# Performance work log

Measured on AMD Instinct MI355X. Metric: run time of the kernel, lower is better.

The kernel has to match this reference:

```python
import jax, jax.numpy as jnp
import numpy as np

B, T, D = 2, 2048, 2048
NH, NKV = 16, 4
HD = D // NH  # 128
BASE, TSL = 10000.0, 1024


def rotary_tables(T, hd, base=BASE, tsl=TSL):
    # Matches Rotary.forward with rd == hd (rd=0 in __init__ -> full head dim).
    ar = jnp.arange(0, hd, 2, dtype=jnp.float32) / hd
    if T <= tsl:
        inv = 1.0 / (base ** ar)
    else:
        # NTK-style rescale; note right-assoc exponent in original torch code:
        # 1/(base * (T/tsl) ** ((rd/(rd-2)) ** ar))
        inv = 1.0 / (base * jnp.power(T / tsl, jnp.power(hd / (hd - 2.0), ar)))
    f = jnp.outer(jnp.arange(T, dtype=jnp.float32), inv)  # [T, hd//2]
    cos = jnp.cos(f)[None, :, None, :]  # [1,T,1,hd//2]
    sin = jnp.sin(f)[None, :, None, :]
    return cos, sin


def apply_rope(x, cos, sin):
    # full-dim rope: split halves, rotate
    h = x.shape[-1] // 2
    x1, x2 = x[..., :h], x[..., h:]
    return jnp.concatenate((x1 * cos + x2 * sin, -x1 * sin + x2 * cos), axis=-1)


def rms_norm(x):
    eps = jnp.finfo(x.dtype).eps
    return x * jax.lax.rsqrt(jnp.mean(x * x, axis=-1, keepdims=True) + eps)


def setup_inputs() -> dict:
    key = jax.random.key(0)
    k0, k1, k2, k3, k4 = jax.random.split(key, 5)
    s = 0.02
    return {
        "x": jax.random.normal(k0, (B, T, D), jnp.float32),
        "qw": jax.random.normal(k1, (NH * HD, D), jnp.float32) * s,
        "kw": jax.random.normal(k2, (NKV * HD, D), jnp.float32) * s,
        "vw": jax.random.normal(k3, (NKV * HD, D), jnp.float32) * s,
        "ow": jax.random.normal(k4, (D, D), jnp.float32) * s,
        "qg": jnp.ones((NH,), jnp.float32),
    }


def reference(x, qw, kw, vw, ow, qg):
    Bx, Tx, Dx = x.shape
    q = (x @ qw.T).reshape(Bx, Tx, NH, HD)
    k = (x @ kw.T).reshape(Bx, Tx, NKV, HD)
    v = (x @ vw.T).reshape(Bx, Tx, NKV, HD)
    q = rms_norm(q)
    k = rms_norm(k)
    cos, sin = rotary_tables(Tx, HD)
    q = apply_rope(q, cos, sin) * qg[None, None, :, None]
    k = apply_rope(k, cos, sin)
    # GQA: repeat kv heads
    r = NH // NKV
    k = jnp.repeat(k, r, axis=2)  # [B,T,NH,HD]
    v = jnp.repeat(v, r, axis=2)
    scale = 1.0 / jnp.sqrt(jnp.asarray(HD, q.dtype))
    scores = jnp.einsum("bqhd,bkhd->bhqk", q, k) * scale  # [B,NH,T,T]
    causal = jnp.tril(jnp.ones((Tx, Tx), dtype=bool))
    scores = jnp.where(causal[None, None, :, :], scores, jnp.asarray(-jnp.inf, scores.dtype))
    attn = jax.nn.softmax(scores, axis=-1)
    y = jnp.einsum("bhqk,bkhd->bqhd", attn, v)  # [B,T,NH,HD]
    return y.reshape(Bx, Tx, Dx) @ ow.T
```

## Files before the change

kernel.cpp:

```cpp
#include <hip/hip_runtime.h>
#include <hip/hip_bf16.h>
#include <stdint.h>


typedef __attribute__((ext_vector_type(8))) short short8;
typedef __attribute__((ext_vector_type(4))) float f32x4;

#define GLOAD16(gp, lp) \
  __builtin_amdgcn_global_load_lds((const __attribute__((address_space(1))) void*)(gp), \
                                   (__attribute__((address_space(3))) void*)(lp), 16, 0, 0)

__device__ __forceinline__ float bf2f(unsigned short u) {
  union { unsigned int i; float f; } v; v.i = ((unsigned int)u) << 16; return v.f;
}
__device__ __forceinline__ unsigned short f2bf(float f) {
  union { float fl; unsigned int i; } v; v.fl = f;
  unsigned int r = v.i + 0x7fffu + ((v.i >> 16) & 1u);
  return (unsigned short)(r >> 16);
}

__global__ __launch_bounds__(256) void prep_kernel(
    const float* __restrict__ x, const float* __restrict__ qw,
    const float* __restrict__ kw, const float* __restrict__ vw,
    const float* __restrict__ ow,
    unsigned short* __restrict__ xb, unsigned short* __restrict__ wqkv,
    unsigned short* __restrict__ owb, float* __restrict__ cost, float* __restrict__ sint) {
  const int NX = 2097152;
  const int NW = 1572864;
  const int NO = 1048576;
  const int NT = 131072;
  int tid = blockIdx.x * 256 + threadIdx.x;
  if (tid < NX) {
    float4 v = ((const float4*)x)[tid];
    uint2 o; o.x = (unsigned)f2bf(v.x) | ((unsigned)f2bf(v.y) << 16);
    o.y = (unsigned)f2bf(v.z) | ((unsigned)f2bf(v.w) << 16);
    ((uint2*)xb)[tid] = o;
  } else if (tid < NX + NW) {
    int i = tid - NX; int e = i * 4;
    const float* src = (e < 4194304) ? (qw + e)
                     : (e < 5242880) ? (kw + (e - 4194304))
                                     : (vw + (e - 5242880));
    float4 v = *(const float4*)src;
    uint2 o; o.x = (unsigned)f2bf(v.x) | ((unsigned)f2bf(v.y) << 16);
    o.y = (unsigned)f2bf(v.z) | ((unsigned)f2bf(v.w) << 16);
    ((uint2*)wqkv)[i] = o;
  } else if (tid < NX + NW + NO) {
    int i = tid - NX - NW;
    float4 v = ((const float4*)ow)[i];
    uint2 o; o.x = (unsigned)f2bf(v.x) | ((unsigned)f2bf(v.y) << 16);
    o.y = (unsigned)f2bf(v.z) | ((unsigned)f2bf(v.w) << 16);
    ((uint2*)owb)[i] = o;
  } else if (tid < NX + NW + NO + NT) {
    int i = tid - NX - NW - NO;
    int t = i >> 6, j = i & 63;
    float e = exp2f(0.02272008f * (float)j * (1.0f / 64.0f));
    float inv = 1.0f / (10000.0f * exp2f(e));
    float f = (float)t * inv;
    cost[i] = cosf(f);
    sint[i] = sinf(f);
  }
}

template <int OUTF>
__global__ __launch_bounds__(256) void gemm_bt(const unsigned short* __restrict__ A,
                                               const unsigned short* __restrict__ Bw,
                                               void* __restrict__ Cp,
                                               int M, int N, int K) {
  __shared__ unsigned short a_sm[128 * 64];
  __shared__ unsigned short b_sm[128 * 64];
  const int tid = threadIdx.x;
  const int l = tid & 63, w = tid >> 6;
  const int lane_r = l & 15, lane_g = l >> 4;
  const int wr = w >> 1, wc = w & 1;
  const int m0 = blockIdx.y * 128, n0 = blockIdx.x * 128;

  f32x4 acc[4][4];
#pragma unroll
  for (int i = 0; i < 4; ++i)
#pragma unroll
    for (int j = 0; j < 4; ++j) acc[i][j] = {0.f, 0.f, 0.f, 0.f};

  const unsigned short* gA[4]; const unsigned short* gB[4];
  unsigned short* lA[4]; unsigned short* lB[4];
#pragma unroll
  for (int t = 0; t < 4; ++t) {
    int idx = t * 256 + tid;
    int row = idx >> 3, c = idx & 7;
    int gc = c ^ (row & 7);
    gA[t] = A + (size_t)(m0 + row) * K + gc * 8;
    gB[t] = Bw + (size_t)(n0 + row) * K + gc * 8;
    lA[t] = &a_sm[idx * 8];
    lB[t] = &b_sm[idx * 8];
  }
  int oA[2][4], oB[2][4];
#pragma unroll
  for (int ks = 0; ks < 2; ++ks)
#pragma unroll
    for (int i = 0; i < 4; ++i) {
      int ra = wr * 64 + i * 16 + lane_r;
      oA[ks][i] = ((ra * 64 + ks * 32 + lane_g * 8) * 2) ^ ((ra & 7) << 4);
      int rb = wc * 64 + i * 16 + lane_r;
      oB[ks][i] = ((rb * 64 + ks * 32 + lane_g * 8) * 2) ^ ((rb & 7) << 4);
    }

  for (int kt = 0; kt < K; kt += 64) {
#pragma unroll
    for (int t = 0; t < 4; ++t) {
      GLOAD16(gA[t] + kt, lA[t]);
      GLOAD16(gB[t] + kt, lB[t]);
    }
    __syncthreads();
#pragma unroll
    for (int ks = 0; ks < 2; ++ks) {
      short8 af[4], bfr[4];
#pragma unroll
      for (int i = 0; i < 4; ++i) {
        af[i] = *(const short8*)((const char*)a_sm + oA[ks][i]);
        bfr[i] = *(const short8*)((const char*)b_sm + oB[ks][i]);
      }
#pragma unroll
      for (int i = 0; i < 4; ++i)
#pragma unroll
        for (int j = 0; j < 4; ++j)
          acc[i][j] = __builtin_amdgcn_mfma_f32_16x16x32_bf16(af[i], bfr[j], acc[i][j], 0, 0, 0);
    }
    __syncthreads();
  }
#pragma unroll
  for (int i = 0; i < 4; ++i) {
    int row = m0 + wr * 64 + i * 16 + lane_g * 4;
#pragma unroll
    for (int j = 0; j < 4; ++j) {
      int col = n0 + wc * 64 + j * 16 + lane_r;
#pragma unroll
      for (int r = 0; r < 4; ++r) {
        float v = acc[i][j][r];
        if (OUTF)
          ((float*)Cp)[(size_t)(row + r) * N + col] = v;
        else
          ((unsigned short*)Cp)[(size_t)(row + r) * N + col] = f2bf(v);
      }
    }
  }
}

__global__ __launch_bounds__(256) void normrope_kernel(unsigned short* __restrict__ qkv,
                                                       const float* __restrict__ cost,
                                                       const float* __restrict__ sint,
                                                       const float* __restrict__ qg) {
  const int tid = threadIdx.x, l = tid & 63, w = tid >> 6;
  int row = blockIdx.x * 4 + w;
  int tok = row / 20, hh = row - tok * 20;
  int t = tok & 2047;
  bool isq = hh < 16;
  int col0 = isq ? hh * 128 : 2048 + (hh - 16) * 128;
  unsigned short* p = qkv + (size_t)tok * 3072 + col0 + 2 * l;
  unsigned int u = *(const unsigned int*)p;
  float x0 = bf2f((unsigned short)(u & 0xffffu));
  float x1 = bf2f((unsigned short)(u >> 16));
  float ss = x0 * x0 + x1 * x1;
#pragma unroll
  for (int m = 1; m < 64; m <<= 1) ss += __shfl_xor(ss, m);
  float rn = rsqrtf(ss * (1.0f / 128.0f) + 1.1920928955078125e-07f);
  float n0 = x0 * rn, n1 = x1 * rn;
  float p0 = __shfl_xor(n0, 32);
  float p1 = __shfl_xor(n1, 32);
  int jj = (2 * l) & 63;
  float c0 = cost[t * 64 + jj], c1 = cost[t * 64 + jj + 1];
  float s0 = sint[t * 64 + jj], s1 = sint[t * 64 + jj + 1];
  float o0, o1;
  if (l < 32) { o0 = n0 * c0 + p0 * s0; o1 = n1 * c1 + p1 * s1; }
  else        { o0 = -p0 * s0 + n0 * c0; o1 = -p1 * s1 + n1 * c1; }
  if (isq) { float g = qg[hh] * 0.08838834764831845f; o0 *= g; o1 *= g; }
  *(unsigned int*)p = (unsigned)f2bf(o0) | ((unsigned)f2bf(o1) << 16);
}

__global__ __launch_bounds__(256) void vtrans_kernel(const unsigned short* __restrict__ qkv,
                                                     unsigned short* __restrict__ vtg) {
  __shared__ unsigned short tile[64][132];
  int bid = blockIdx.x;
  int pan = bid & 7, tt = bid >> 3;
  int b = pan >> 2, kvh = pan & 3;
  int t0 = tt * 64;
  const unsigned short* src = qkv + ((size_t)(b * 2048 + t0)) * 3072 + 2560 + kvh * 128;
#pragma unroll
  for (int i = 0; i < 8; ++i) {
    int idx = i * 256 + threadIdx.x;
    int row = idx >> 5, c4 = idx & 31;
    uint2 v = *(const uint2*)(src + (size_t)row * 3072 + c4 * 4);
    *(uint2*)&tile[row][c4 * 4] = v;
  }
  __syncthreads();
  unsigned short* dst = vtg + (size_t)pan * 262144 + t0;
#pragma unroll
  for (int i = 0; i < 8; ++i) {
    int idx = i * 256 + threadIdx.x;
    int d = idx >> 4, tc = idx & 15;
    unsigned short a0 = tile[tc * 4 + 0][d], a1 = tile[tc * 4 + 1][d];
    unsigned short a2 = tile[tc * 4 + 2][d], a3 = tile[tc * 4 + 3][d];
    uint2 o; o.x = (unsigned)a0 | ((unsigned)a1 << 16);
    o.y = (unsigned)a2 | ((unsigned)a3 << 16);
    *(uint2*)(dst + (size_t)d * 2048 + tc * 4) = o;
  }
}

__global__ __launch_bounds__(512) void attn_fa4(const unsigned short* __restrict__ qkv,
                                                const unsigned short* __restrict__ vtg,
                                                unsigned short* __restrict__ y) {
  extern __shared__ char smc[];
  const int tid = threadIdx.x;
  const int l = tid & 63, w = tid >> 6;
  const int lane_r = l & 15, lane_g = l >> 4;

  int n = blockIdx.x;
  int pan = n & 7;
  int b = pan >> 2, kvh = pan & 3;
  int idx2 = n >> 3;
  int h = kvh * 4 + (idx2 & 3);
  int pairIdx = idx2 >> 2;
  const size_t rowbase = (size_t)b * 2048;
  const unsigned short* kvK = qkv + rowbase * 3072;
  const unsigned short* vtp = vtg + (size_t)pan * 262144;

  int kg[2], vg[2], sl[2];
#pragma unroll
  for (int t = 0; t < 2; ++t) {
    int idx = t * 512 + tid;
    { int row = idx >> 4, c = idx & 15, gc = c ^ (row & 7);
      kg[t] = row * 3072 + 2048 + kvh * 128 + gc * 8; }
    { int d = idx >> 3, c = idx & 7, gc = c ^ (d & 7);
      vg[t] = d * 2048 + gc * 8; }
    sl[t] = idx * 16;
  }
  const int swz = (lane_r & 7) << 4;
  int oK[4][4];
#pragma unroll
  for (int ct = 0; ct < 4; ++ct)
#pragma unroll
    for (int ks = 0; ks < 4; ++ks)
      oK[ct][ks] = ((ct * 16 + lane_r) * 256 + ks * 64 + lane_g * 16) ^ swz;
  int oV[2][8];
#pragma unroll
  for (int kk = 0; kk < 2; ++kk)
#pragma unroll
    for (int dt = 0; dt < 8; ++dt)
      oV[kk][dt] = ((dt * 16 + lane_r) * 128 + kk * 64 + lane_g * 16) ^ swz;
  const int pbase = 65536 + w * 2048;
  int pw_off[4];
#pragma unroll
  for (int ct = 0; ct < 4; ++ct)
    pw_off[ct] = pbase + lane_r * 128 + ((ct * 32 + lane_g * 8) ^ swz);
  int pr_off[2];
#pragma unroll
  for (int kk = 0; kk < 2; ++kk)
    pr_off[kk] = pbase + lane_r * 128 + ((kk * 64 + lane_g * 16) ^ swz);

  auto STAGE = [&](int tile, int bufsel) {
    const unsigned short* srcK = kvK + (size_t)tile * 64 * 3072;
    const unsigned short* srcV = vtp + tile * 64;
    char* kd = smc + bufsel * 16384;
    char* vd = smc + 32768 + bufsel * 16384;
#pragma unroll
    for (int t = 0; t < 2; ++t) {
      GLOAD16(srcK + kg[t], kd + sl[t]);
      GLOAD16(srcV + vg[t], vd + sl[t]);
    }
  };

#pragma unroll 1
  for (int phase = 0; phase < 2; ++phase) {
    const int qt = phase ? pairIdx : 15 - pairIdx;
    const int q0 = qt * 128;
    const int nkb = 2 * qt + 2;
    const int wrow0 = q0 + w * 16;
    const int qrow = wrow0 + lane_r;

    STAGE(0, 0);
    short8 qf[4];
#pragma unroll
    for (int ks = 0; ks < 4; ++ks)
      qf[ks] = *(const short8*)(qkv + (rowbase + qrow) * 3072 + h * 128 + ks * 32 + lane_g * 8);

    f32x4 acc[8];
#pragma unroll
    for (int dt = 0; dt < 8; ++dt) acc[dt] = {0.f, 0.f, 0.f, 0.f};
    float mrun = -1e30f, lrun = 0.f;

    __syncthreads();

#pragma unroll 1
    for (int kb = 0; kb < nkb; ++kb) {
      const int cur = kb & 1;
      if (kb + 1 < nkb) STAGE(kb + 1, cur ^ 1);
      const int j0 = kb * 64;
      const bool active = (j0 <= wrow0 + 15);
      if (active) {
        const int kbb = cur * 16384;
        f32x4 s[4];
#pragma unroll
        for (int ct = 0; ct < 4; ++ct) s[ct] = {0.f, 0.f, 0.f, 0.f};
        __builtin_amdgcn_s_setprio(1);
#pragma unroll
        for (int ct = 0; ct < 4; ++ct)
#pragma unroll
          for (int ks = 0; ks < 4; ++ks) {
            short8 kf = *(const short8*)(smc + kbb + oK[ct][ks]);
            s[ct] = __builtin_amdgcn_mfma_f32_16x16x32_bf16(kf, qf[ks], s[ct], 0, 0, 0);
          }
        __builtin_amdgcn_s_setprio(0);
        if (j0 + 63 > wrow0) {
#pragma unroll
          for (int ct = 0; ct < 4; ++ct) {
            int kg0 = j0 + ct * 16 + lane_g * 4;
#pragma unroll
            for (int r = 0; r < 4; ++r)
              if (kg0 + r > qrow) s[ct][r] = -1e30f;
          }
        }
        float mx = s[0][0];
#pragma unroll
        for (int ct = 0; ct < 4; ++ct)
#pragma unroll
          for (int r = 0; r < 4; ++r) mx = fmaxf(mx, s[ct][r]);
        mx = fmaxf(mx, __shfl_xor(mx, 16));
        mx = fmaxf(mx, __shfl_xor(mx, 32));
        float mn = fmaxf(mrun, mx);
        float corr = __expf(mrun - mn);
        mrun = mn;
        float rs = 0.f;
#pragma unroll
        for (int ct = 0; ct < 4; ++ct)
#pragma unroll
          for (int r = 0; r < 4; ++r) {
            float e = __expf(s[ct][r] - mn);
            s[ct][r] = e; rs += e;
          }
        rs += __shfl_xor(rs, 16);
        rs += __shfl_xor(rs, 32);
        lrun = lrun * corr + rs;
#pragma unroll
        for (int ct = 0; ct < 4; ++ct) {
          uint2 pv;
          pv.x = (unsigned)f2bf(s[ct][0]) | ((unsigned)f2bf(s[ct][1]) << 16);
          pv.y = (unsigned)f2bf(s[ct][2]) | ((unsigned)f2bf(s[ct][3]) << 16);
          *(uint2*)(smc + pw_off[ct]) = pv;
        }
#pragma unroll
        for (int dt = 0; dt < 8; ++dt)
#pragma unroll
          for (int r = 0; r < 4; ++r) acc[dt][r] *= corr;
        short8 pf[2];
        pf[0] = *(const short8*)(smc + pr_off[0]);
        pf[1] = *(const short8*)(smc + pr_off[1]);
        const int vbase = 32768 + cur * 16384;
        __builtin_amdgcn_s_setprio(1);
#pragma unroll
        for (int kk = 0; kk < 2; ++kk)
#pragma unroll
          for (int dt = 0; dt < 8; ++dt) {
            short8 vf = *(const short8*)(smc + vbase + oV[kk][dt]);
            acc[dt] = __builtin_amdgcn_mfma_f32_16x16x32_bf16(vf, pf[kk], acc[dt], 0, 0, 0);
          }
        __builtin_amdgcn_s_setprio(0);
      }
      __syncthreads();
    }
    float linv = 1.0f / lrun;
    unsigned short* yrow = y + (rowbase + qrow) * 2048 + h * 128;
#pragma unroll
    for (int dt = 0; dt < 8; ++dt) {
      uint2 o;
      o.x = (unsigned)f2bf(acc[dt][0] * linv) | ((unsigned)f2bf(acc[dt][1] * linv) << 16);
      o.y = (unsigned)f2bf(acc[dt][2] * linv) | ((unsigned)f2bf(acc[dt][3] * linv) << 16);
      *(uint2*)(yrow + dt * 16 + lane_g * 4) = o;
    }
  }
}

extern "C" void kernel_launch(void* const* d_in, const int* in_sizes, int n_in,
                              void* d_out, int out_size, void* d_ws, size_t ws_size,
                              hipStream_t stream) {
  (void)in_sizes; (void)n_in; (void)out_size; (void)ws_size;
  const float* x  = (const float*)d_in[0];
  const float* qw = (const float*)d_in[1];
  const float* kw = (const float*)d_in[2];
  const float* vw = (const float*)d_in[3];
  const float* ow = (const float*)d_in[4];
  const float* qg = (const float*)d_in[5];

  char* ws = (char*)d_ws;
  unsigned short* xb   = (unsigned short*)(ws + 0);
  unsigned short* vtg  = (unsigned short*)(ws + 0);
  unsigned short* wqkv = (unsigned short*)(ws + 16777216);
  unsigned short* owb  = (unsigned short*)(ws + 29360128);
  unsigned short* qkvb = (unsigned short*)(ws + 37748736);
  unsigned short* y    = (unsigned short*)(ws + 62914560);
  float* cost          = (float*)(ws + 79691776);
  float* sint          = (float*)(ws + 80216064);

  prep_kernel<<<18944, 256, 0, stream>>>(x, qw, kw, vw, ow, xb, wqkv, owb, cost, sint);
  gemm_bt<0><<<dim3(3072 / 128, 4096 / 128), 256, 0, stream>>>(xb, wqkv, qkvb, 4096, 3072, 2048);
  normrope_kernel<<<20480, 256, 0, stream>>>(qkvb, cost, sint, qg);
  vtrans_kernel<<<256, 256, 0, stream>>>(qkvb, vtg);
  attn_fa4<<<256, 512, 81920, stream>>>(qkvb, vtg, y);
  gemm_bt<1><<<dim3(2048 / 128, 4096 / 128), 256, 0, stream>>>(y, owb, d_out, 4096, 2048, 2048);
}
```

Baseline: 228.0 us.

## Replace GEMM with 256x128-tile, 512-thread, triple-buffered pipelined kernel

Replaces the simple single-buffered 128x128 bf16 GEMM with a 256x128-tile, 8-wave kernel. It uses a three-stage LDS ring with global_load_lds prefetch two K-steps ahead, manual vmcnt waits and a single barrier per step. Workgroup IDs are remapped in chunks of eight, apparently to improve cache locality across CUs. MFMA sections run at raised priority. The goal is to hide global load latency and remove the per-iteration double barrier, at the cost of 144KB dynamic LDS per block, which allows only one block per CU.

```diff
diff --git a/kernel.cpp b/kernel.cpp
--- a/kernel.cpp
+++ b/kernel.cpp
@@ -62,17 +62,22 @@
 }
 
 template <int OUTF>
-__global__ __launch_bounds__(256) void gemm_bt(const unsigned short* __restrict__ A,
-                                               const unsigned short* __restrict__ Bw,
-                                               void* __restrict__ Cp,
-                                               int M, int N, int K) {
-  __shared__ unsigned short a_sm[128 * 64];
-  __shared__ unsigned short b_sm[128 * 64];
+__global__ __launch_bounds__(512) void gemm_bt2(const unsigned short* __restrict__ A,
+                                                const unsigned short* __restrict__ Bw,
+                                                void* __restrict__ Cp,
+                                                int MT, int NT, int N, int K) {
+  extern __shared__ char smc[];
   const int tid = threadIdx.x;
   const int l = tid & 63, w = tid >> 6;
   const int lane_r = l & 15, lane_g = l >> 4;
   const int wr = w >> 1, wc = w & 1;
-  const int m0 = blockIdx.y * 128, n0 = blockIdx.x * 128;
+
+  int nwg = MT * NT, qch = nwg >> 3;
+  int orig = blockIdx.x;
+  int wgid = (orig & 7) * qch + (orig >> 3);
+  int by = wgid % MT;
+  int bx = wgid / MT;
+  const int m0 = by * 256, n0 = bx * 128;
 
   f32x4 acc[4][4];
 #pragma unroll
@@ -80,51 +85,71 @@
 #pragma unroll
     for (int j = 0; j < 4; ++j) acc[i][j] = {0.f, 0.f, 0.f, 0.f};
 
-  const unsigned short* gA[4]; const unsigned short* gB[4];
-  unsigned short* lA[4]; unsigned short* lB[4];
+  const unsigned short* gA[4]; int lA[4];
 #pragma unroll
   for (int t = 0; t < 4; ++t) {
-    int idx = t * 256 + tid;
-    int row = idx >> 3, c = idx & 7;
-    int gc = c ^ (row & 7);
+    int idx = t * 512 + tid;
+    int row = idx >> 3, c = idx & 7, gc = c ^ (row & 7);
     gA[t] = A + (size_t)(m0 + row) * K + gc * 8;
+    lA[t] = idx * 16;
+  }
+  const unsigned short* gB[2]; int lB[2];
+#pragma unroll
+  for (int t = 0; t < 2; ++t) {
+    int idx = t * 512 + tid;
+    int row = idx >> 3, c = idx & 7, gc = c ^ (row & 7);
     gB[t] = Bw + (size_t)(n0 + row) * K + gc * 8;
-    lA[t] = &a_sm[idx * 8];
-    lB[t] = &b_sm[idx * 8];
-  }
-  int oA[2][4], oB[2][4];
-#pragma unroll
-  for (int ks = 0; ks < 2; ++ks)
-#pragma unroll
-    for (int i = 0; i < 4; ++i) {
+    lB[t] = idx * 16;
+  }
+  int oA[4][2], oB[4][2];
+#pragma unroll
+  for (int i = 0; i < 4; ++i)
+#pragma unroll
+    for (int ks = 0; ks < 2; ++ks) {
       int ra = wr * 64 + i * 16 + lane_r;
-      oA[ks][i] = ((ra * 64 + ks * 32 + lane_g * 8) * 2) ^ ((ra & 7) << 4);
+      oA[i][ks] = (ra * 128 + ks * 64 + lane_g * 16) ^ ((ra & 7) << 4);
       int rb = wc * 64 + i * 16 + lane_r;
-      oB[ks][i] = ((rb * 64 + ks * 32 + lane_g * 8) * 2) ^ ((rb & 7) << 4);
+      oB[i][ks] = (rb * 128 + ks * 64 + lane_g * 16) ^ ((rb & 7) << 4);
     }
 
-  for (int kt = 0; kt < K; kt += 64) {
-#pragma unroll
-    for (int t = 0; t < 4; ++t) {
-      GLOAD16(gA[t] + kt, lA[t]);
-      GLOAD16(gB[t] + kt, lB[t]);
-    }
-    __syncthreads();
-#pragma unroll
-    for (int ks = 0; ks < 2; ++ks) {
-      short8 af[4], bfr[4];
-#pragma unroll
-      for (int i = 0; i < 4; ++i) {
-        af[i] = *(const short8*)((const char*)a_sm + oA[ks][i]);
-        bfr[i] = *(const short8*)((const char*)b_sm + oB[ks][i]);
+  auto STAGE = [&](int kt, int bsel) {
+    char* kd = smc + bsel * 49152;
+    char* bd = kd + 32768;
+#pragma unroll
+    for (int t = 0; t < 4; ++t) GLOAD16(gA[t] + kt, kd + lA[t]);
+#pragma unroll
+    for (int t = 0; t < 2; ++t) GLOAD16(gB[t] + kt, bd + lB[t]);
+  };
+
+  const int NS = K >> 6;
+  STAGE(0, 0);
+  STAGE(64, 1);
+#pragma unroll 1
+  for (int s = 0; s < NS; ++s) {
+    if (s + 1 < NS) asm volatile("s_waitcnt vmcnt(6)" ::: "memory");
+    else            asm volatile("s_waitcnt vmcnt(0)" ::: "memory");
+    __builtin_amdgcn_s_barrier();
+    __builtin_amdgcn_sched_barrier(0);
+    if (s + 2 < NS) STAGE((s + 2) * 64, (s + 2) % 3);
+    const char* ab = smc + (s % 3) * 49152;
+    const char* bb = ab + 32768;
+    short8 af[4][2], bf[4][2];
+#pragma unroll
+    for (int i = 0; i < 4; ++i)
+#pragma unroll
+      for (int ks = 0; ks < 2; ++ks) {
+        af[i][ks] = *(const short8*)(ab + oA[i][ks]);
+        bf[i][ks] = *(const short8*)(bb + oB[i][ks]);
       }
-#pragma unroll
-      for (int i = 0; i < 4; ++i)
-#pragma unroll
-        for (int j = 0; j < 4; ++j)
-          acc[i][j] = __builtin_amdgcn_mfma_f32_16x16x32_bf16(af[i], bfr[j], acc[i][j], 0, 0, 0);
-    }
-    __syncthreads();
+    __builtin_amdgcn_s_setprio(1);
+#pragma unroll
+    for (int i = 0; i < 4; ++i)
+#pragma unroll
+      for (int j = 0; j < 4; ++j)
+#pragma unroll
+        for (int ks = 0; ks < 2; ++ks)
+          acc[i][j] = __builtin_amdgcn_mfma_f32_16x16x32_bf16(af[i][ks], bf[j][ks], acc[i][j], 0, 0, 0);
+    __builtin_amdgcn_s_setprio(0);
   }
 #pragma unroll
   for (int i = 0; i < 4; ++i) {
@@ -399,9 +424,9 @@
   float* sint          = (float*)(ws + 80216064);
 
   prep_kernel<<<18944, 256, 0, stream>>>(x, qw, kw, vw, ow, xb, wqkv, owb, cost, sint);
-  gemm_bt<0><<<dim3(3072 / 128, 4096 / 128), 256, 0, stream>>>(xb, wqkv, qkvb, 4096, 3072, 2048);
+  gemm_bt2<0><<<384, 512, 147456, stream>>>(xb, wqkv, qkvb, 16, 24, 3072, 2048);
   normrope_kernel<<<20480, 256, 0, stream>>>(qkvb, cost, sint, qg);
   vtrans_kernel<<<256, 256, 0, stream>>>(qkvb, vtg);
   attn_fa4<<<256, 512, 81920, stream>>>(qkvb, vtg, y);
-  gemm_bt<1><<<dim3(2048 / 128, 4096 / 128), 256, 0, stream>>>(y, owb, d_out, 4096, 2048, 2048);
-}
+  gemm_bt2<1><<<256, 512, 147456, stream>>>(y, owb, d_out, 16, 16, 2048, 2048);
+}
```

After: 214.4 us. 6.0% less time.
